# Kernel optimization log

Measured on AMD Instinct MI355X. Metric: run time of the kernel, lower is better.

Reference implementation:

```python
import jax, jax.numpy as jnp
import numpy as np

N, T, E, H, V = 32768, 20, 50, 50, 200
PAD = 0

def setup_inputs() -> dict:
    key = jax.random.key(0)
    ks = jax.random.split(key, 11)
    s = 1.0 / np.sqrt(H)  # torch LSTM init scale
    return {
        "char_indices": jax.random.randint(ks[0], (N, T), 0, V, dtype=jnp.int32),
        "word_lengths": jax.random.randint(ks[1], (N,), 0, T + 1, dtype=jnp.int32),
        "emb": jax.random.normal(ks[2], (V, E), jnp.float32) * 0.1,
        "W_ih_f": jax.random.normal(ks[3], (4 * H, E), jnp.float32) * s,
        "W_hh_f": jax.random.normal(ks[4], (4 * H, H), jnp.float32) * s,
        "b_ih_f": jax.random.normal(ks[5], (4 * H,), jnp.float32) * s,
        "b_hh_f": jax.random.normal(ks[6], (4 * H,), jnp.float32) * s,
        "W_ih_b": jax.random.normal(ks[7], (4 * H, E), jnp.float32) * s,
        "W_hh_b": jax.random.normal(ks[8], (4 * H, H), jnp.float32) * s,
        "b_ih_b": jax.random.normal(ks[9], (4 * H,), jnp.float32) * s,
        "b_hh_b": jax.random.normal(ks[10], (4 * H,), jnp.float32) * s,
    }

def _run_dir(x, lengths, W_ih, W_hh, b_ih, b_hh, reverse):
    # x: [N,T,E]; returns final hidden state [N,H] at the word's true boundary.
    n = x.shape[0]
    xg = jnp.einsum('nte,ge->ntg', x, W_ih) + b_ih + b_hh  # [N,T,4H]
    def step(carry, t):
        h, c = carry
        g = xg[:, t] + h @ W_hh.T  # [N,4H]
        i, f, gg, o = jnp.split(g, 4, axis=-1)
        c_new = jax.nn.sigmoid(f) * c + jax.nn.sigmoid(i) * jnp.tanh(gg)
        h_new = jax.nn.sigmoid(o) * jnp.tanh(c_new)
        valid = (t < lengths)[:, None]  # only update inside the word
        return (jnp.where(valid, h_new, h), jnp.where(valid, c_new, c)), None
    ts = jnp.arange(T - 1, -1, -1) if reverse else jnp.arange(T)
    z = jnp.zeros((n, W_hh.shape[1]), x.dtype)
    (h, _), _ = jax.lax.scan(step, (z, z), ts)
    return h

def reference(char_indices, word_lengths, emb, W_ih_f, W_hh_f, b_ih_f, b_hh_f,
              W_ih_b, W_hh_b, b_ih_b, b_hh_b):
    emb = emb.at[PAD].set(0.0)  # padding_idx row is zero
    x = emb[char_indices]  # [N,T,E]
    h_f = _run_dir(x, word_lengths, W_ih_f, W_hh_f, b_ih_f, b_hh_f, reverse=False)
    h_b = _run_dir(x, word_lengths, W_ih_b, W_hh_b, b_ih_b, b_hh_b, reverse=True)
    return jnp.concatenate([h_f, h_b], axis=-1)  # [N, 2H]
```

## Files before the change

### kernel.cpp

```cpp
#include <hip/hip_runtime.h>


#define TT    20
#define HH    50
#define VV    200
#define TILES 13
#define GSTR  212
#define GSH   (VV * GSTR)
#define WSH   (TILES * 16 * 64)
#define NW    32768
#define NB_G  50
#define NB_W  104
#define NB_H  128
#define NBLK  4096

#define N2LOG2E (-1.4426950408889634f)
#define P2LOG2E 2.8853900817779268f

typedef __attribute__((ext_vector_type(8))) short bf16x8;
typedef __attribute__((ext_vector_type(4))) float f32x4;

__device__ __forceinline__ float frcp(float x) { return __builtin_amdgcn_rcpf(x); }
#if __has_builtin(__builtin_amdgcn_exp2f)
__device__ __forceinline__ float fexp2(float x) { return __builtin_amdgcn_exp2f(x); }
#else
__device__ __forceinline__ float fexp2(float x) { return exp2f(x); }
#endif

__device__ __forceinline__ short f2bf(float x) {
    unsigned b = __builtin_bit_cast(unsigned, x);
    unsigned r = (b + 0x7FFFu + ((b >> 16) & 1u)) >> 16;
    return (short)r;
}
__device__ __forceinline__ float bfhi(unsigned w) {
    return __builtin_bit_cast(float, w & 0xFFFF0000u);
}
__device__ __forceinline__ float bflo(unsigned w) {
    return __builtin_bit_cast(float, w << 16);
}

__global__ void k_prep(const float* __restrict__ emb,
                       const float* __restrict__ Wih_f, const float* __restrict__ bih_f,
                       const float* __restrict__ bhh_f,
                       const float* __restrict__ Wih_b, const float* __restrict__ bih_b,
                       const float* __restrict__ bhh_b,
                       const float* __restrict__ Whh_f, const float* __restrict__ Whh_b,
                       const int* __restrict__ lens,
                       short* __restrict__ Gimg, short* __restrict__ Wimg,
                       int* __restrict__ cnt) {
    int blk = blockIdx.x;
    int tid = threadIdx.x;
    __shared__ float Wl[4 * HH * HH];
    __shared__ float bs[4 * HH];

    if (blk < NB_G) {
        int d = blk / 25;
        int vbase = (blk % 25) * 8;
        const float* Wih = d ? Wih_b : Wih_f;
        const float* bih = d ? bih_b : bih_f;
        const float* bhh = d ? bhh_b : bhh_f;
        for (int i = tid; i < 4 * HH * HH; i += 256) {
            int r = i / HH;
            float sc = (r / HH == 2) ? P2LOG2E : N2LOG2E;
            Wl[i] = Wih[i] * sc;
        }
        if (tid < 4 * HH) {
            float sc = (tid / HH == 2) ? P2LOG2E : N2LOG2E;
            bs[tid] = (bih[tid] + bhh[tid]) * sc;
        }
        __syncthreads();
        int r = tid;
        if (r < 4 * HH) {
            int g = r / HH, u = r % HH;
            #pragma unroll
            for (int vv = 0; vv < 8; ++vv) {
                int v = vbase + vv;
                float s = bs[r];
                if (v != 0) {
                    #pragma unroll 10
                    for (int e = 0; e < HH; ++e)
                        s = fmaf(emb[v * HH + e], Wl[r * HH + e], s);
                }
                Gimg[d * GSH + v * GSTR + u * 4 + g] = f2bf(s);
            }
        } else {
            for (int k = r - 4 * HH; k < 8 * 12; k += 56) {
                int v = vbase + k / 12;
                Gimg[d * GSH + v * GSTR + 4 * HH + (k % 12)] = 0;
            }
        }
    } else if (blk < NB_G + NB_W) {
        int idx = (blk - NB_G) * 256 + tid;
        if (idx >= 2 * WSH) return;
        int d = idx / WSH;
        int e = idx % WSH;
        int t = e >> 10, m = (e >> 6) & 15, k = e & 63;
        int u = 4 * t + (m >> 2), g = m & 3;
        const float* Whh = d ? Whh_b : Whh_f;
        float sc = (g == 2) ? P2LOG2E : N2LOG2E;
        float val = (k < HH && u < HH) ? Whh[(g * HH + u) * HH + k] * sc : 0.0f;
        int ksw = (k & 7) | (((k >> 3) ^ (m & 7)) << 3);
        Wimg[d * WSH + (e & ~63) + ksw] = f2bf(val);
    } else {
        int hb = blk - NB_G - NB_W;
        __shared__ int hcnt[21];
        if (tid < 21) hcnt[tid] = 0;
        __syncthreads();
        atomicAdd(&hcnt[lens[hb * 256 + tid]], 1);
        __syncthreads();
        if (tid < 21) cnt[hb * 21 + tid] = hcnt[tid];
    }
}

__global__ void k_scat(const int* __restrict__ lens, const int* __restrict__ cnt,
                       int* __restrict__ perm) {
    __shared__ int lcnt[NB_H * 21];
    __shared__ int part[8][21];
    __shared__ int tot[21];
    __shared__ int cur[21];
    int b = blockIdx.x, t = threadIdx.x;
    for (int i = t; i < NB_H * 21; i += 256) lcnt[i] = cnt[i];
    __syncthreads();
    if (t < 168) {
        int L = t % 21, c = t / 21;
        int s = 0;
        for (int bb = c * 16; bb < c * 16 + 16; ++bb) s += lcnt[bb * 21 + L];
        part[c][L] = s;
    }
    __syncthreads();
    if (t < 21) {
        int a = 0;
        #pragma unroll
        for (int c = 0; c < 8; ++c) a += part[c][t];
        tot[t] = a;
    }
    __syncthreads();
    if (t < 21) {
        int a = 0;
        for (int L2 = 20; L2 > t; --L2) a += tot[L2];
        for (int bb = 0; bb < b; ++bb) a += lcnt[bb * 21 + t];
        cur[t] = a;
    }
    __syncthreads();
    int i = b * 256 + t;
    int pos = atomicAdd(&cur[lens[i]], 1);
    perm[pos] = i;
}

__launch_bounds__(128, 4)
__global__ void k_lstm(const int* __restrict__ chars, const int* __restrict__ lens,
                       const int* __restrict__ perm,
                       const short* __restrict__ Gimg, const short* __restrict__ Wimg,
                       float* __restrict__ out) {
    __shared__ __align__(16) short hs[2][1024];
    __shared__ unsigned short cs[16 * TT];

    int gb   = blockIdx.x;
    int d    = gb & 1;
    int grp  = gb >> 1;
    int tid  = threadIdx.x;
    int lane = tid & 63;
    int wv   = __builtin_amdgcn_readfirstlane(tid >> 6);
    int quad = lane >> 4;
    int n    = lane & 15;
    int x7   = n & 7;
    int slotbase = grp * 16;

    {
        int4 z = {0, 0, 0, 0};
        int4* hz = (int4*)&hs[0][0];
        hz[tid] = z;
        hz[tid + 128] = z;
    }
    for (int i = tid; i < 16 * TT; i += 128) {
        int w = perm[slotbase + i / TT];
        cs[i] = (unsigned short)(chars[w * TT + i % TT] * GSTR);
    }

    int word = perm[slotbase + n];
    int L = lens[word];
    int mL = L;
    #pragma unroll
    for (int off = 8; off; off >>= 1) {
        int t2 = __shfl_xor(mL, off);
        mL = mL > t2 ? mL : t2;
    }
    mL = __builtin_amdgcn_readfirstlane(mL);

    int pa0 = quad ^ x7;
    int pa1 = (quad + 4) ^ x7;
    int tbase = wv * 6;
    int u0 = 4 * tbase + quad;

    const short* Wd = Wimg + d * WSH;
    bf16x8 A0[7], A1[7];
    #pragma unroll
    for (int tt = 0; tt < 7; ++tt) {
        int t = tbase + tt;
        A0[tt] = *(const bf16x8*)(Wd + (t * 16 + n) * 64 + pa0 * 8);
        A1[tt] = *(const bf16x8*)(Wd + (t * 16 + n) * 64 + pa1 * 8);
    }
    int hidx[7];
    #pragma unroll
    for (int tt = 0; tt < 7; ++tt) {
        int uu = u0 + 4 * tt;
        hidx[tt] = n * 64 + (((uu >> 3) ^ x7) << 3) + (uu & 7);
    }

    const short* Gq = Gimg + d * GSH + quad * 4 + tbase * 16;
    const unsigned short* cw = cs + n * TT;

    float cst[7], hf[7];
    #pragma unroll
    for (int tt = 0; tt < 7; ++tt) { cst[tt] = 0.0f; hf[tt] = 0.0f; }

    __syncthreads();

    int vcur = cw[(d && L > 0) ? (L - 1) : 0];
    int cur = 0;

    #pragma unroll 1
    for (int s = 0; s < mL; ++s) {
        bool valid = s < L;

        const short* hb = hs[cur];
        bf16x8 B0 = *(const bf16x8*)(hb + n * 64 + pa0 * 8);
        bf16x8 B1 = *(const bf16x8*)(hb + n * 64 + pa1 * 8);

        int sn = s + 1;
        int pn = (sn < L) ? (d ? (L - 1 - sn) : sn) : 0;
        int vnxt = cw[pn];

        const int2* gp = (const int2*)(Gq + vcur);
        short* hnb = hs[cur ^ 1];

        #pragma unroll
        for (int tt = 0; tt < 7; ++tt) {
            int2 gw = gp[tt * 4];
            f32x4 a;
            a[0] = bflo((unsigned)gw.x);
            a[1] = bfhi((unsigned)gw.x);
            a[2] = bflo((unsigned)gw.y);
            a[3] = bfhi((unsigned)gw.y);
            a = __builtin_amdgcn_mfma_f32_16x16x32_bf16(A0[tt], B0, a, 0, 0, 0);
            a = __builtin_amdgcn_mfma_f32_16x16x32_bf16(A1[tt], B1, a, 0, 0, 0);

            float ig = frcp(1.0f + fexp2(a[0]));
            float fg = frcp(1.0f + fexp2(a[1]));
            float tg = 1.0f - 2.0f * frcp(1.0f + fexp2(a[2]));
            float og = frcp(1.0f + fexp2(a[3]));
            float cn = fg * cst[tt] + ig * tg;
            float hn = og * (1.0f - 2.0f * frcp(1.0f + fexp2(cn * P2LOG2E)));

            int uu = u0 + 4 * tt;
            bool upd = valid && (uu < HH);
            cst[tt] = upd ? cn : cst[tt];
            hf[tt]  = upd ? hn : hf[tt];
            if (uu < HH) hnb[hidx[tt]] = f2bf(hf[tt]);
        }

        vcur = vnxt;
        __syncthreads();
        cur ^= 1;
    }

    float* orow = out + (size_t)word * (2 * HH) + d * HH;
    #pragma unroll
    for (int tt = 0; tt < 7; ++tt) {
        int uu = u0 + 4 * tt;
        if (uu < HH) orow[uu] = hf[tt];
    }
}

extern "C" void kernel_launch(void* const* d_in, const int* in_sizes, int n_in,
                              void* d_out, int out_size, void* d_ws, size_t ws_size,
                              hipStream_t stream) {
    const int*   chars = (const int*)d_in[0];
    const int*   lens  = (const int*)d_in[1];
    const float* emb   = (const float*)d_in[2];
    const float* Wih_f = (const float*)d_in[3];
    const float* Whh_f = (const float*)d_in[4];
    const float* bih_f = (const float*)d_in[5];
    const float* bhh_f = (const float*)d_in[6];
    const float* Wih_b = (const float*)d_in[7];
    const float* Whh_b = (const float*)d_in[8];
    const float* bih_b = (const float*)d_in[9];
    const float* bhh_b = (const float*)d_in[10];
    float* out = (float*)d_out;

    short* Gimg = (short*)d_ws;
    short* Wimg = Gimg + 2 * GSH;
    int*   cnt  = (int*)(Wimg + 2 * WSH);
    int*   perm = cnt + NB_H * 21;

    k_prep<<<NB_G + NB_W + NB_H, 256, 0, stream>>>(emb, Wih_f, bih_f, bhh_f,
                                                   Wih_b, bih_b, bhh_b,
                                                   Whh_f, Whh_b, lens,
                                                   Gimg, Wimg, cnt);
    k_scat<<<NB_H, 256, 0, stream>>>(lens, cnt, perm);
    k_lstm<<<NBLK, 128, 0, stream>>>(chars, lens, perm, Gimg, Wimg, out);
}
```

Measured before the change: 163.9 us.

## Give each wave its own 16-word group and stage recurrent weights in LDS

Before, two waves split the 13 gate tiles for one 16-word group, exchanged the hidden state through double-buffered LDS, and hit a block barrier at every timestep. Now each of four waves in a 256-thread block owns its own 16-word group and computes all 13 tiles. It updates its private hidden-state buffer in place, so the per-step __syncthreads goes away. The recurrent weight image is copied into LDS once per block and re-read from LDS for every step. This trades register-resident weights and the barrier for extra LDS reads, a longer serial chain of tiles per wave, and more register pressure from 13 accumulators.

```diff
diff --git a/kernel.cpp b/kernel.cpp
--- a/kernel.cpp
+++ b/kernel.cpp
@@ -12,7 +12,7 @@
 #define NB_G  50
 #define NB_W  104
 #define NB_H  128
-#define NBLK  4096
+#define NBLK  1024
 
 #define N2LOG2E (-1.4426950408889634f)
 #define P2LOG2E 2.8853900817779268f
@@ -147,36 +147,44 @@
     perm[pos] = i;
 }
 
-__launch_bounds__(128, 4)
+__launch_bounds__(256, 4)
 __global__ void k_lstm(const int* __restrict__ chars, const int* __restrict__ lens,
                        const int* __restrict__ perm,
                        const short* __restrict__ Gimg, const short* __restrict__ Wimg,
                        float* __restrict__ out) {
-    __shared__ __align__(16) short hs[2][1024];
-    __shared__ unsigned short cs[16 * TT];
+    __shared__ __align__(16) short Wa[WSH];
+    __shared__ __align__(16) short hs[4][1024];
+    __shared__ unsigned short cs[4 * 16 * TT];
 
     int gb   = blockIdx.x;
     int d    = gb & 1;
-    int grp  = gb >> 1;
+    int g4   = gb >> 1;
+    int slot0 = g4 * 64;
     int tid  = threadIdx.x;
     int lane = tid & 63;
     int wv   = __builtin_amdgcn_readfirstlane(tid >> 6);
     int quad = lane >> 4;
     int n    = lane & 15;
     int x7   = n & 7;
-    int slotbase = grp * 16;
-
+
+    {
+        const int4* src = (const int4*)(Wimg + d * WSH);
+        int4* dst = (int4*)Wa;
+        for (int i = tid; i < WSH / 8; i += 256) dst[i] = src[i];
+    }
     {
         int4 z = {0, 0, 0, 0};
         int4* hz = (int4*)&hs[0][0];
         hz[tid] = z;
-        hz[tid + 128] = z;
-    }
-    for (int i = tid; i < 16 * TT; i += 128) {
-        int w = perm[slotbase + i / TT];
+        hz[tid + 256] = z;
+    }
+    for (int i = tid; i < 64 * TT; i += 256) {
+        int w = perm[slot0 + i / TT];
         cs[i] = (unsigned short)(chars[w * TT + i % TT] * GSTR);
     }
-
+    __syncthreads();
+
+    int slotbase = slot0 + wv * 16;
     int word = perm[slotbase + n];
     int L = lens[word];
     int mL = L;
@@ -189,85 +197,70 @@
 
     int pa0 = quad ^ x7;
     int pa1 = (quad + 4) ^ x7;
-    int tbase = wv * 6;
-    int u0 = 4 * tbase + quad;
-
-    const short* Wd = Wimg + d * WSH;
-    bf16x8 A0[7], A1[7];
+
+    const bf16x8* ap = (const bf16x8*)Wa;
+    short* hw = hs[wv];
+    const unsigned short* cw = cs + wv * 16 * TT + n * TT;
+    const short* Gq = Gimg + d * GSH + quad * 4;
+
+    float cst[TILES], hf[TILES];
     #pragma unroll
-    for (int tt = 0; tt < 7; ++tt) {
-        int t = tbase + tt;
-        A0[tt] = *(const bf16x8*)(Wd + (t * 16 + n) * 64 + pa0 * 8);
-        A1[tt] = *(const bf16x8*)(Wd + (t * 16 + n) * 64 + pa1 * 8);
-    }
-    int hidx[7];
-    #pragma unroll
-    for (int tt = 0; tt < 7; ++tt) {
-        int uu = u0 + 4 * tt;
-        hidx[tt] = n * 64 + (((uu >> 3) ^ x7) << 3) + (uu & 7);
-    }
-
-    const short* Gq = Gimg + d * GSH + quad * 4 + tbase * 16;
-    const unsigned short* cw = cs + n * TT;
-
-    float cst[7], hf[7];
-    #pragma unroll
-    for (int tt = 0; tt < 7; ++tt) { cst[tt] = 0.0f; hf[tt] = 0.0f; }
-
-    __syncthreads();
+    for (int t = 0; t < TILES; ++t) { cst[t] = 0.0f; hf[t] = 0.0f; }
 
     int vcur = cw[(d && L > 0) ? (L - 1) : 0];
-    int cur = 0;
 
     #pragma unroll 1
     for (int s = 0; s < mL; ++s) {
         bool valid = s < L;
 
-        const short* hb = hs[cur];
-        bf16x8 B0 = *(const bf16x8*)(hb + n * 64 + pa0 * 8);
-        bf16x8 B1 = *(const bf16x8*)(hb + n * 64 + pa1 * 8);
+        bf16x8 B0 = *(const bf16x8*)(hw + n * 64 + pa0 * 8);
+        bf16x8 B1 = *(const bf16x8*)(hw + n * 64 + pa1 * 8);
 
         int sn = s + 1;
         int pn = (sn < L) ? (d ? (L - 1 - sn) : sn) : 0;
         int vnxt = cw[pn];
 
         const int2* gp = (const int2*)(Gq + vcur);
-        short* hnb = hs[cur ^ 1];
-
+
+        f32x4 acc[TILES];
         #pragma unroll
-        for (int tt = 0; tt < 7; ++tt) {
+        for (int tt = 0; tt < TILES; ++tt) {
             int2 gw = gp[tt * 4];
             f32x4 a;
             a[0] = bflo((unsigned)gw.x);
             a[1] = bfhi((unsigned)gw.x);
             a[2] = bflo((unsigned)gw.y);
             a[3] = bfhi((unsigned)gw.y);
-            a = __builtin_amdgcn_mfma_f32_16x16x32_bf16(A0[tt], B0, a, 0, 0, 0);
-            a = __builtin_amdgcn_mfma_f32_16x16x32_bf16(A1[tt], B1, a, 0, 0, 0);
-
-            float ig = frcp(1.0f + fexp2(a[0]));
-            float fg = frcp(1.0f + fexp2(a[1]));
-            float tg = 1.0f - 2.0f * frcp(1.0f + fexp2(a[2]));
-            float og = frcp(1.0f + fexp2(a[3]));
+            bf16x8 A0 = ap[(tt * 16 + n) * 8 + pa0];
+            bf16x8 A1 = ap[(tt * 16 + n) * 8 + pa1];
+            a = __builtin_amdgcn_mfma_f32_16x16x32_bf16(A0, B0, a, 0, 0, 0);
+            a = __builtin_amdgcn_mfma_f32_16x16x32_bf16(A1, B1, a, 0, 0, 0);
+            acc[tt] = a;
+        }
+        #pragma unroll
+        for (int tt = 0; tt < TILES; ++tt) {
+            float ig = frcp(1.0f + fexp2(acc[tt][0]));
+            float fg = frcp(1.0f + fexp2(acc[tt][1]));
+            float tg = 1.0f - 2.0f * frcp(1.0f + fexp2(acc[tt][2]));
+            float og = frcp(1.0f + fexp2(acc[tt][3]));
             float cn = fg * cst[tt] + ig * tg;
             float hn = og * (1.0f - 2.0f * frcp(1.0f + fexp2(cn * P2LOG2E)));
-
-            int uu = u0 + 4 * tt;
+            int uu = 4 * tt + quad;
             bool upd = valid && (uu < HH);
             cst[tt] = upd ? cn : cst[tt];
             hf[tt]  = upd ? hn : hf[tt];
-            if (uu < HH) hnb[hidx[tt]] = f2bf(hf[tt]);
-        }
-
+            if (upd) {
+                int hidx = n * 64 + (((tt >> 1) ^ x7) << 3) + (tt & 1) * 4 + quad;
+                hw[hidx] = f2bf(hn);
+            }
+        }
         vcur = vnxt;
-        __syncthreads();
-        cur ^= 1;
     }
 
     float* orow = out + (size_t)word * (2 * HH) + d * HH;
     #pragma unroll
-    for (int tt = 0; tt < 7; ++tt) {
-        int uu = u0 + 4 * tt;
+    for (int tt = 0; tt < TILES; ++tt) {
+        int uu = 4 * tt + quad;
         if (uu < HH) orow[uu] = hf[tt];
     }
 }
@@ -298,5 +291,5 @@
                                                    Whh_f, Whh_b, lens,
                                                    Gimg, Wimg, cnt);
     k_scat<<<NB_H, 256, 0, stream>>>(lens, cnt, perm);
-    k_lstm<<<NBLK, 128, 0, stream>>>(chars, lens, perm, Gimg, Wimg, out);
-}
+    k_lstm<<<NBLK, 256, 0, stream>>>(chars, lens, perm, Gimg, Wimg, out);
+}
```

New measurement: 317.2 us. +93.5%, slower.

## Split LSTM tiles across four waves and flatten gate-table precompute

Applied to the files above, without the earlier changes.

The recurrent kernel now runs 256 threads per block, with 4 waves covering the 13 gate tiles (4/3/3/3) instead of 2 waves each covering 7. Recurrent weight fragments are reloaded from global memory every step instead of being held in registers. The gate-table precompute is flattened to one output element per thread across many more blocks, dropping the shared-memory staging. This shortens the per-step critical path and adds parallelism, at the cost of repeated weight loads, more barrier participants per step, and occupancy now capped by launch bounds of one block.

```diff
diff --git a/kernel.cpp b/kernel.cpp
--- a/kernel.cpp
+++ b/kernel.cpp
@@ -9,7 +9,7 @@
 #define GSH   (VV * GSTR)
 #define WSH   (TILES * 16 * 64)
 #define NW    32768
-#define NB_G  50
+#define NB_G  332
 #define NB_W  104
 #define NB_H  128
 #define NBLK  4096
@@ -50,45 +50,26 @@
                        int* __restrict__ cnt) {
     int blk = blockIdx.x;
     int tid = threadIdx.x;
-    __shared__ float Wl[4 * HH * HH];
-    __shared__ float bs[4 * HH];
-
     if (blk < NB_G) {
-        int d = blk / 25;
-        int vbase = (blk % 25) * 8;
+        int idx = blk * 256 + tid;
+        if (idx >= 2 * GSH) return;
+        int d = idx / GSH;
+        int rem = idx % GSH;
+        int v = rem / GSTR;
+        int u = (rem % GSTR) >> 2;
+        int g = idx & 3;
+        if (u >= HH) { Gimg[idx] = 0; return; }
+        int r = g * HH + u;
         const float* Wih = d ? Wih_b : Wih_f;
         const float* bih = d ? bih_b : bih_f;
         const float* bhh = d ? bhh_b : bhh_f;
-        for (int i = tid; i < 4 * HH * HH; i += 256) {
-            int r = i / HH;
-            float sc = (r / HH == 2) ? P2LOG2E : N2LOG2E;
-            Wl[i] = Wih[i] * sc;
+        float s = bih[r] + bhh[r];
+        if (v != 0) {
+            #pragma unroll 10
+            for (int e = 0; e < HH; ++e) s = fmaf(emb[v * HH + e], Wih[r * HH + e], s);
         }
-        if (tid < 4 * HH) {
-            float sc = (tid / HH == 2) ? P2LOG2E : N2LOG2E;
-            bs[tid] = (bih[tid] + bhh[tid]) * sc;
-        }
-        __syncthreads();
-        int r = tid;
-        if (r < 4 * HH) {
-            int g = r / HH, u = r % HH;
-            #pragma unroll
-            for (int vv = 0; vv < 8; ++vv) {
-                int v = vbase + vv;
-                float s = bs[r];
-                if (v != 0) {
-                    #pragma unroll 10
-                    for (int e = 0; e < HH; ++e)
-                        s = fmaf(emb[v * HH + e], Wl[r * HH + e], s);
-                }
-                Gimg[d * GSH + v * GSTR + u * 4 + g] = f2bf(s);
-            }
-        } else {
-            for (int k = r - 4 * HH; k < 8 * 12; k += 56) {
-                int v = vbase + k / 12;
-                Gimg[d * GSH + v * GSTR + 4 * HH + (k % 12)] = 0;
-            }
-        }
+        float sc = (g == 2) ? P2LOG2E : N2LOG2E;
+        Gimg[idx] = f2bf(s * sc);
     } else if (blk < NB_G + NB_W) {
         int idx = (blk - NB_G) * 256 + tid;
         if (idx >= 2 * WSH) return;
@@ -147,7 +128,7 @@
     perm[pos] = i;
 }
 
-__launch_bounds__(128, 4)
+__launch_bounds__(256, 1)
 __global__ void k_lstm(const int* __restrict__ chars, const int* __restrict__ lens,
                        const int* __restrict__ perm,
                        const short* __restrict__ Gimg, const short* __restrict__ Wimg,
@@ -168,11 +149,9 @@
 
     {
         int4 z = {0, 0, 0, 0};
-        int4* hz = (int4*)&hs[0][0];
-        hz[tid] = z;
-        hz[tid + 128] = z;
-    }
-    for (int i = tid; i < 16 * TT; i += 128) {
+        ((int4*)&hs[0][0])[tid] = z;
+    }
+    for (int i = tid; i < 16 * TT; i += 256) {
         int w = perm[slotbase + i / TT];
         cs[i] = (unsigned short)(chars[w * TT + i % TT] * GSTR);
     }
@@ -189,30 +168,29 @@
 
     int pa0 = quad ^ x7;
     int pa1 = (quad + 4) ^ x7;
-    int tbase = wv * 6;
-    int u0 = 4 * tbase + quad;
+
+    int tb = (wv == 0) ? 0 : (4 + 3 * (wv - 1));
+    int nt = (wv == 0) ? 4 : 3;
 
     const short* Wd = Wimg + d * WSH;
-    bf16x8 A0[7], A1[7];
-    #pragma unroll
-    for (int tt = 0; tt < 7; ++tt) {
-        int t = tbase + tt;
-        A0[tt] = *(const bf16x8*)(Wd + (t * 16 + n) * 64 + pa0 * 8);
-        A1[tt] = *(const bf16x8*)(Wd + (t * 16 + n) * 64 + pa1 * 8);
-    }
-    int hidx[7];
-    #pragma unroll
-    for (int tt = 0; tt < 7; ++tt) {
-        int uu = u0 + 4 * tt;
-        hidx[tt] = n * 64 + (((uu >> 3) ^ x7) << 3) + (uu & 7);
-    }
-
-    const short* Gq = Gimg + d * GSH + quad * 4 + tbase * 16;
+    const short* Gq = Gimg + d * GSH + quad * 4;
     const unsigned short* cw = cs + n * TT;
 
-    float cst[7], hf[7];
-    #pragma unroll
-    for (int tt = 0; tt < 7; ++tt) { cst[tt] = 0.0f; hf[tt] = 0.0f; }
+    int uu[4], hidx[4];
+    const short* Ap0[4];
+    const short* Ap1[4];
+    #pragma unroll
+    for (int tt = 0; tt < 4; ++tt) {
+        int tg = tb + tt;
+        uu[tt] = 4 * tg + quad;
+        hidx[tt] = n * 64 + (((uu[tt] >> 3) ^ x7) << 3) + (uu[tt] & 7);
+        Ap0[tt] = Wd + (tg * 16 + n) * 64 + pa0 * 8;
+        Ap1[tt] = Wd + (tg * 16 + n) * 64 + pa1 * 8;
+    }
+
+    float cst[4], hf[4];
+    #pragma unroll
+    for (int tt = 0; tt < 4; ++tt) { cst[tt] = 0.0f; hf[tt] = 0.0f; }
 
     __syncthreads();
 
@@ -235,28 +213,32 @@
         short* hnb = hs[cur ^ 1];
 
         #pragma unroll
-        for (int tt = 0; tt < 7; ++tt) {
-            int2 gw = gp[tt * 4];
-            f32x4 a;
-            a[0] = bflo((unsigned)gw.x);
-            a[1] = bfhi((unsigned)gw.x);
-            a[2] = bflo((unsigned)gw.y);
-            a[3] = bfhi((unsigned)gw.y);
-            a = __builtin_amdgcn_mfma_f32_16x16x32_bf16(A0[tt], B0, a, 0, 0, 0);
-            a = __builtin_amdgcn_mfma_f32_16x16x32_bf16(A1[tt], B1, a, 0, 0, 0);
-
-            float ig = frcp(1.0f + fexp2(a[0]));
-            float fg = frcp(1.0f + fexp2(a[1]));
-            float tg = 1.0f - 2.0f * frcp(1.0f + fexp2(a[2]));
-            float og = frcp(1.0f + fexp2(a[3]));
-            float cn = fg * cst[tt] + ig * tg;
-            float hn = og * (1.0f - 2.0f * frcp(1.0f + fexp2(cn * P2LOG2E)));
-
-            int uu = u0 + 4 * tt;
-            bool upd = valid && (uu < HH);
-            cst[tt] = upd ? cn : cst[tt];
-            hf[tt]  = upd ? hn : hf[tt];
-            if (uu < HH) hnb[hidx[tt]] = f2bf(hf[tt]);
+        for (int tt = 0; tt < 4; ++tt) {
+            if (tt < nt) {
+                int tg = tb + tt;
+                int2 gw = gp[tg * 4];
+                f32x4 a;
+                a[0] = bflo((unsigned)gw.x);
+                a[1] = bfhi((unsigned)gw.x);
+                a[2] = bflo((unsigned)gw.y);
+                a[3] = bfhi((unsigned)gw.y);
+                bf16x8 A0 = *(const bf16x8*)Ap0[tt];
+                bf16x8 A1 = *(const bf16x8*)Ap1[tt];
+                a = __builtin_amdgcn_mfma_f32_16x16x32_bf16(A0, B0, a, 0, 0, 0);
+                a = __builtin_amdgcn_mfma_f32_16x16x32_bf16(A1, B1, a, 0, 0, 0);
+
+                float ig = frcp(1.0f + fexp2(a[0]));
+                float fg = frcp(1.0f + fexp2(a[1]));
+                float tg2 = 1.0f - 2.0f * frcp(1.0f + fexp2(a[2]));
+                float og = frcp(1.0f + fexp2(a[3]));
+                float cn = fg * cst[tt] + ig * tg2;
+                float hn = og * (1.0f - 2.0f * frcp(1.0f + fexp2(cn * P2LOG2E)));
+
+                bool upd = valid && (uu[tt] < HH);
+                cst[tt] = upd ? cn : cst[tt];
+                hf[tt]  = upd ? hn : hf[tt];
+                if (uu[tt] < HH) hnb[hidx[tt]] = f2bf(hf[tt]);
+            }
         }
 
         vcur = vnxt;
@@ -266,9 +248,8 @@
 
     float* orow = out + (size_t)word * (2 * HH) + d * HH;
     #pragma unroll
-    for (int tt = 0; tt < 7; ++tt) {
-        int uu = u0 + 4 * tt;
-        if (uu < HH) orow[uu] = hf[tt];
+    for (int tt = 0; tt < 4; ++tt) {
+        if (tt < nt && uu[tt] < HH) orow[uu[tt]] = hf[tt];
     }
 }
 
@@ -298,5 +279,5 @@
                                                    Whh_f, Whh_b, lens,
                                                    Gimg, Wimg, cnt);
     k_scat<<<NB_H, 256, 0, stream>>>(lens, cnt, perm);
-    k_lstm<<<NBLK, 128, 0, stream>>>(chars, lens, perm, Gimg, Wimg, out);
-}
+    k_lstm<<<NBLK, 256, 0, stream>>>(chars, lens, perm, Gimg, Wimg, out);
+}
```

New measurement: 153.8 us. 6.2% less time.
